# Performance work log

Hardware: AMD Instinct MI355X
Metric: run time of the kernel (lower is better)

Reference implementation:

```python
import jax, jax.numpy as jnp
import numpy as np

B, T, D = 2, 4096, 2048
HK, HV = 16, 32            # key heads, value heads (gqa_factor = 2)
AK, UV = 128, 128          # key head dim A, value head dim U
KEY_DIM = HK * AK          # 2048
VALUE_DIM = HV * UV        # 4096
CONV_DIM = 2 * KEY_DIM + VALUE_DIM  # 8192
KCONV = 4
CHUNK = 64
EPS = 1e-6


def setup_inputs() -> dict:
    key = jax.random.key(0)
    ks = jax.random.split(key, 10)
    s = lambda d: 1.0 / np.sqrt(d)
    return {
        "hidden": jax.random.normal(ks[0], (B, T, D), jnp.float32),
        "W_qkv": jax.random.normal(ks[1], (D, CONV_DIM), jnp.float32) * s(D),
        "W_z": jax.random.normal(ks[2], (D, VALUE_DIM), jnp.float32) * s(D),
        "W_b": jax.random.normal(ks[3], (D, HV), jnp.float32) * s(D),
        "W_a": jax.random.normal(ks[4], (D, HV), jnp.float32) * s(D),
        "conv_weight": jax.random.normal(ks[5], (CONV_DIM, KCONV), jnp.float32) * s(KCONV),
        "dt_bias": jnp.ones((HV,), jnp.float32),
        "A_log": jnp.log(jax.random.uniform(ks[6], (HV,), jnp.float32) * 16.0 + 1e-4),
        "norm_w": jnp.ones((UV,), jnp.float32),
        "W_out": jax.random.normal(ks[7], (VALUE_DIM, D), jnp.float32) * s(VALUE_DIM),
    }


def _l2norm(x, eps=1e-6):
    return x * jax.lax.rsqrt((x * x).sum(axis=-1, keepdims=True) + eps)


def _chunk_gated_delta_rule(q, k, v, g, beta, chunk_size=CHUNK):
    # inputs: q,k (B,T,Hv,A) l2-normalized below; v (B,T,Hv,U); g,beta (B,T,Hv)
    q = _l2norm(q)
    k = _l2norm(k)
    q, k, v = [x.transpose(0, 2, 1, 3).astype(jnp.float32) for x in (q, k, v)]
    beta = beta.transpose(0, 2, 1).astype(jnp.float32)
    g = g.transpose(0, 2, 1).astype(jnp.float32)
    Bs, H, Tt, A = k.shape
    U = v.shape[-1]
    pad = (chunk_size - Tt % chunk_size) % chunk_size
    if pad:
        q = jnp.pad(q, ((0, 0), (0, 0), (0, pad), (0, 0)))
        k = jnp.pad(k, ((0, 0), (0, 0), (0, pad), (0, 0)))
        v = jnp.pad(v, ((0, 0), (0, 0), (0, pad), (0, 0)))
        beta = jnp.pad(beta, ((0, 0), (0, 0), (0, pad)))
        g = jnp.pad(g, ((0, 0), (0, 0), (0, pad)))
    total = Tt + pad
    J = total // chunk_size
    q = q * (A ** -0.5)
    vb = v * beta[..., None]
    kb = k * beta[..., None]
    rs = lambda x, d: x.reshape(Bs, H, J, chunk_size, d)
    qj, kj, kbj = rs(q, A), rs(k, A), rs(kb, A)
    vbj = rs(vb, U)
    gj = jnp.cumsum(g.reshape(Bs, H, J, chunk_size), axis=-1)
    tril = jnp.tril(jnp.ones((chunk_size, chunk_size), jnp.float32))
    decay = jnp.exp((gj[..., :, None] - gj[..., None, :]) * tril) * tril
    upper = jnp.triu(jnp.ones((chunk_size, chunk_size), bool))
    attn = -(jnp.einsum('BHJLA,BHJMA->BHJLM', kbj, kj) * decay)
    attn = jnp.where(upper, 0.0, attn)

    def correction_step(i, a):  # sequential UT transform over rows
        row = a[..., i, :]
        return a.at[..., i, :].set(row + jnp.einsum('...j,...jk->...k', row, a))

    attn = jax.lax.fori_loop(1, chunk_size, correction_step, attn)
    attn = attn + jnp.eye(chunk_size, dtype=jnp.float32)
    v_corr = jnp.einsum('BHJLM,BHJMU->BHJLU', attn, vbj)
    k_cd = jnp.einsum('BHJLM,BHJMA->BHJLA', attn, kbj * jnp.exp(gj)[..., None])
    upper1 = jnp.triu(jnp.ones((chunk_size, chunk_size), bool), k=1)

    def chunk_step(st, j):  # st: (B,H,A,U) recurrent state
        qc, kc = qj[:, :, j], kj[:, :, j]
        vc, gc, kcd = v_corr[:, :, j], gj[:, :, j], k_cd[:, :, j]
        dm = decay[:, :, j]
        intra = jnp.einsum('BHLA,BHMA->BHLM', qc, kc) * dm
        intra = jnp.where(upper1, 0.0, intra)
        v_new = vc - jnp.einsum('BHLA,BHAU->BHLU', kcd, st)
        inter = jnp.exp(gc)[..., None] * jnp.einsum('BHLA,BHAU->BHLU', qc, st)
        out_c = inter + jnp.einsum('BHLM,BHMU->BHLU', intra, v_new)
        k_dec = kc * jnp.exp(gc[:, :, -1:] - gc)[..., None]
        st = st * jnp.exp(gc[:, :, -1])[..., None, None] + jnp.einsum('BHMA,BHMU->BHAU', k_dec, v_new)
        return st, out_c

    st0 = jnp.zeros((Bs, H, A, U), jnp.float32)
    _, outs = jax.lax.scan(chunk_step, st0, jnp.arange(J))
    out = outs.transpose(1, 2, 0, 3, 4).reshape(Bs, H, total, U)[:, :, :Tt]
    return out.transpose(0, 2, 1, 3)  # (B,T,H,U)


def _forward(hidden, W_qkv, W_z, W_b, W_a, conv_weight, dt_bias, A_log, norm_w, W_out):
    Bs, Tl, _ = hidden.shape
    mixed = (hidden @ W_qkv).transpose(0, 2, 1)  # (B, C, T)
    z = hidden @ W_z                              # (B, T, value_dim)
    b = hidden @ W_b                              # (B, T, Hv)
    a = hidden @ W_a                              # (B, T, Hv)
    # causal depthwise conv1d (kernel KCONV) + SiLU
    xp = jnp.pad(mixed, ((0, 0), (0, 0), (KCONV - 1, 0)))
    conv = sum(conv_weight[None, :, kk:kk + 1] * xp[:, :, kk:kk + Tl] for kk in range(KCONV))
    mixed = jax.nn.silu(conv).transpose(0, 2, 1)  # (B, T, C)
    q, k, v = jnp.split(mixed, [KEY_DIM, 2 * KEY_DIM], axis=-1)
    q = q.reshape(Bs, Tl, HK, AK)
    k = k.reshape(Bs, Tl, HK, AK)
    v = v.reshape(Bs, Tl, HV, UV)
    beta = jax.nn.sigmoid(b)
    g = -jnp.exp(A_log.astype(jnp.float32)) * jax.nn.softplus(a.astype(jnp.float32) + dt_bias)
    gqa = HV // HK
    q = jnp.repeat(q, gqa, axis=2)  # matches broadcast_to+reshape interleaving
    k = jnp.repeat(k, gqa, axis=2)
    core = _chunk_gated_delta_rule(q, k, v, g, beta)  # (B,T,Hv,U)
    # gated RMSNorm per value head (Mamba2/Qwen3-Next style: gate then norm)
    x = core.reshape(-1, UV)
    zf = z.reshape(-1, UV).astype(jnp.float32)
    xg = x * jax.nn.silu(zf)
    normed = norm_w * (xg * jax.lax.rsqrt((xg * xg).mean(-1, keepdims=True) + EPS))
    return normed.reshape(Bs, Tl, VALUE_DIM).astype(hidden.dtype) @ W_out


def reference(hidden, W_qkv, W_z, W_b, W_a, conv_weight, dt_bias, A_log, norm_w, W_out):
    return _forward(hidden, W_qkv, W_z, W_b, W_a, conv_weight, dt_bias, A_log, norm_w, W_out)
```

## Files before the change

kernel.cpp:

```cpp
#include <hip/hip_runtime.h>

#define B_   2
#define T_   4096
#define D_   2048
#define HV_  32
#define AK_  128
#define UV_  128
#define KD_  2048
#define VD_  4096
#define CD_  8192
#define CHK  64
#define NCH  (T_/CHK)

typedef __attribute__((ext_vector_type(4))) float  f32x4;
typedef __attribute__((ext_vector_type(8))) short  short8;
typedef __attribute__((ext_vector_type(4))) short  short4b;
typedef __attribute__((ext_vector_type(8))) unsigned short u16x8;
typedef __attribute__((ext_vector_type(4))) unsigned short u16x4;

__device__ __forceinline__ float bf2f(unsigned short u) {
  return __uint_as_float(((unsigned)u) << 16);
}
__device__ __forceinline__ unsigned short f2bf(float f) {
  unsigned u = __float_as_uint(f);
  return (unsigned short)((u + 0x7fffu + ((u >> 16) & 1u)) >> 16);
}
__device__ __forceinline__ void gload16(const void* g, void* l) {
  __builtin_amdgcn_global_load_lds((const __attribute__((address_space(1))) void*)g,
                                   (__attribute__((address_space(3))) void*)l, 16, 0, 0);
}

__global__ __launch_bounds__(256) void k_transpose(const float* __restrict__ src,
                                                   unsigned short* __restrict__ dst,
                                                   int K, int N) {
  __shared__ float tile[32][33];
  int k0 = blockIdx.x * 32, n0 = blockIdx.y * 32;
  int tx = threadIdx.x, ty = threadIdx.y;
  #pragma unroll
  for (int i = 0; i < 32; i += 8)
    tile[ty + i][tx] = src[(size_t)(k0 + ty + i) * N + n0 + tx];
  __syncthreads();
  #pragma unroll
  for (int i = 0; i < 32; i += 8)
    dst[(size_t)(n0 + ty + i) * K + k0 + tx] = f2bf(tile[tx][ty + i]);
}

__device__ __forceinline__ void storeC(float* p, float v) { *p = v; }
__device__ __forceinline__ void storeC(unsigned short* p, float v) { *p = f2bf(v); }

template <bool AGL, typename CT>
__global__ __launch_bounds__(256, 2) void k_gemm(const void* __restrict__ Av,
                                                 const unsigned short* __restrict__ BT,
                                                 CT* __restrict__ C, int N, int K) {
  __shared__ __attribute__((aligned(16))) short As[128 * 64];
  __shared__ __attribute__((aligned(16))) short Bs[256 * 64];
  const int tid  = threadIdx.x;
  const int bid  = blockIdx.x;
  const int tb   = bid & 63;
  const size_t bm = (size_t)(8 * (tb & 7) + (tb >> 3)) * 128;
  const size_t bn = (size_t)(bid >> 6) * 256;
  const int lane = tid & 63;
  const int wave = tid >> 6;
  const int wm = (wave >> 1) * 64;
  const int wn = (wave & 1) * 64;
  const int fr = lane & 15;
  const int kg = lane >> 4;
  const int lr = lane >> 3, lc8 = (lane & 7) * 8;
  const short* gb = (const short*)BT + (bn + wave * 64 + lr) * (size_t)K + lc8;
  short* lB = &Bs[wave * 64 * 64];
  const short* gab = (const short*)Av + (bm + wave * 32 + lr) * (size_t)K + lc8;
  short* lA = &As[wave * 32 * 64];

  f32x4 acc[4][8];
  #pragma unroll
  for (int i = 0; i < 4; ++i)
    #pragma unroll
    for (int j2 = 0; j2 < 8; ++j2) acc[i][j2] = (f32x4){0.f, 0.f, 0.f, 0.f};

  for (int kt = 0; kt < K; kt += 64) {
    __syncthreads();
    #pragma unroll
    for (int p = 0; p < 8; ++p)
      gload16(gb + kt + (size_t)(8 * p) * K, lB + (8 * p) * 64);
    if constexpr (AGL) {
      #pragma unroll
      for (int p = 0; p < 4; ++p)
        gload16(gab + kt + (size_t)(8 * p) * K, lA + (8 * p) * 64);
    } else {
      const float* Ag = (const float*)Av + bm * (size_t)K;
      #pragma unroll
      for (int s = 0; s < 8; ++s) {
        int ch = s * 256 + tid;
        int r = ch >> 4, c4 = (ch & 15) * 4;
        float4 v = *(const float4*)(Ag + (size_t)r * K + kt + c4);
        short4b sv = { (short)f2bf(v.x), (short)f2bf(v.y), (short)f2bf(v.z), (short)f2bf(v.w) };
        *(short4b*)&As[r * 64 + c4] = sv;
      }
    }
    __syncthreads();
    #pragma unroll
    for (int kk = 0; kk < 2; ++kk) {
      short8 af[4], bfr[8];
      #pragma unroll
      for (int mi = 0; mi < 4; ++mi) af[mi] = *(const short8*)&As[(wm + mi*16 + fr)*64 + kk*32 + kg*8];
      #pragma unroll
      for (int ni = 0; ni < 4; ++ni) {
        bfr[ni]     = *(const short8*)&Bs[(wn + ni*16 + fr)*64 + kk*32 + kg*8];
        bfr[4 + ni] = *(const short8*)&Bs[(128 + wn + ni*16 + fr)*64 + kk*32 + kg*8];
      }
      #pragma unroll
      for (int mi = 0; mi < 4; ++mi)
        #pragma unroll
        for (int ni = 0; ni < 8; ++ni)
          acc[mi][ni] = __builtin_amdgcn_mfma_f32_16x16x32_bf16(af[mi], bfr[ni], acc[mi][ni], 0, 0, 0);
    }
  }
  #pragma unroll
  for (int mi = 0; mi < 4; ++mi)
    #pragma unroll
    for (int ni = 0; ni < 8; ++ni) {
      size_t row = bm + wm + mi * 16 + kg * 4;
      size_t col = bn + (ni >= 4 ? 128 : 0) + wn + (ni & 3) * 16 + fr;
      #pragma unroll
      for (int e = 0; e < 4; ++e) storeC(&C[(row + e) * (size_t)N + col], acc[mi][ni][e]);
    }
}

__global__ __launch_bounds__(256) void k_beta_g(const float* __restrict__ hidden,
                                                const float* __restrict__ Wb,
                                                const float* __restrict__ Wa,
                                                const float* __restrict__ dt_bias,
                                                const float* __restrict__ A_log,
                                                float* __restrict__ betab,
                                                float* __restrict__ gbuf,
                                                unsigned short* __restrict__ hidb) {
  const int tid = threadIdx.x;
  const int r = tid >> 5, hh = tid & 31;
  const size_t bt = (size_t)blockIdx.x * 8 + r;
  const float* hrow = hidden + bt * D_;
  float sb = 0.f, sa = 0.f;
  for (int d = 0; d < D_; ++d) {
    float hv = hrow[d];
    sb += hv * Wb[d * 32 + hh];
    sa += hv * Wa[d * 32 + hh];
  }
  unsigned short* hb = hidb + bt * D_ + hh * 64;
  #pragma unroll
  for (int d2 = 0; d2 < 64; d2 += 8) {
    float4 v0 = *(const float4*)(hrow + hh * 64 + d2);
    float4 v1 = *(const float4*)(hrow + hh * 64 + d2 + 4);
    u16x8 o = { f2bf(v0.x), f2bf(v0.y), f2bf(v0.z), f2bf(v0.w),
                f2bf(v1.x), f2bf(v1.y), f2bf(v1.z), f2bf(v1.w) };
    *(u16x8*)(hb + d2) = o;
  }
  float beta = 1.f / (1.f + __expf(-sb));
  float xg = sa + dt_bias[hh];
  float sp = (xg > 20.f) ? xg : log1pf(__expf(xg));
  float g = -__expf(A_log[hh]) * sp;
  int b = (int)(bt >> 12);
  int t = (int)(bt & (T_ - 1));
  size_t o = ((size_t)b * HV_ + hh) * T_ + t;
  betab[o] = beta;
  gbuf[o] = g;
}

__global__ __launch_bounds__(256) void k_qkv(const unsigned short* __restrict__ mqk,
                                             const float* __restrict__ cw,
                                             unsigned short* __restrict__ qn,
                                             unsigned short* __restrict__ kn) {
  const int row = blockIdx.x;
  const int b = row >> 12, t = row & (T_ - 1);
  const int tid = threadIdx.x;
  const int c0 = tid * 16;
  float4 w[16];
  #pragma unroll
  for (int e = 0; e < 16; ++e) w[e] = *(const float4*)&cw[(size_t)(c0 + e) * 4];
  float acc[16];
  #pragma unroll
  for (int e = 0; e < 16; ++e) acc[e] = 0.f;
  #pragma unroll
  for (int p = 0; p < 4; ++p) {
    int ts = t - 3 + p;
    if (ts < 0) continue;
    const unsigned short* src = mqk + (size_t)(b * T_ + ts) * 4096 + c0;
    u16x8 v0 = *(const u16x8*)src;
    u16x8 v1 = *(const u16x8*)(src + 8);
    #pragma unroll
    for (int e = 0; e < 8; ++e) {
      acc[e]     += bf2f(v0[e]) * ((const float*)&w[e])[p];
      acc[8 + e] += bf2f(v1[e]) * ((const float*)&w[8 + e])[p];
    }
  }
  float s = 0.f;
  #pragma unroll
  for (int e = 0; e < 16; ++e) {
    float x = acc[e];
    x = x / (1.f + __expf(-x));
    acc[e] = x;
    s += x * x;
  }
  s += __shfl_xor(s, 1); s += __shfl_xor(s, 2); s += __shfl_xor(s, 4);
  float sc = rsqrtf(s + 1e-6f);
  bool isq = (c0 < KD_);
  if (isq) sc *= 0.08838834764831845f;
  int ch = isq ? c0 : (c0 - KD_);
  int hk = ch >> 7, cc = ch & 127;
  unsigned short* dst = (isq ? qn : kn) + ((size_t)(b * 16 + hk) * T_ + t) * 128 + cc;
  u16x8 o0, o1;
  #pragma unroll
  for (int e = 0; e < 8; ++e) { o0[e] = f2bf(acc[e] * sc); o1[e] = f2bf(acc[8 + e] * sc); }
  *(u16x8*)dst = o0;
  *(u16x8*)(dst + 8) = o1;
}

__global__ __launch_bounds__(256) void k_prep(const unsigned short* __restrict__ kn,
                                              const float* __restrict__ gbuf,
                                              const float* __restrict__ betab,
                                              unsigned short* __restrict__ Tg,
                                              unsigned short* __restrict__ knT,
                                              float* __restrict__ gjc) {
  __shared__ __attribute__((aligned(16))) unsigned short kl[CHK][136];
  __shared__ float L[CHK][65];
  __shared__ float W1[CHK][65];
  __shared__ float gj[CHK], bet[CHK];
  const int tid = threadIdx.x;
  const int blk = blockIdx.x;
  const int j = blk & 63, h = (blk >> 6) & 31, b = blk >> 11;
  const int hk = h >> 1;
  const int t0 = j * CHK;
  const int lane = tid & 63, wv = tid >> 6;
  const int fr = lane & 15, kg = lane >> 4;
  const int ty = tid >> 4, tx = tid & 15;

  const unsigned short* ksrc = kn + ((size_t)(b * 16 + hk) * T_ + t0) * 128;
  #pragma unroll
  for (int p = 0; p < 4; ++p) {
    int id = p * 256 + tid;
    int r = id >> 4, c = (id & 15) * 8;
    *(u16x8*)&kl[r][c] = *(const u16x8*)(ksrc + (size_t)r * 128 + c);
  }
  if (tid < 64) {
    float gval = gbuf[((size_t)b * HV_ + h) * T_ + t0 + tid];
    #pragma unroll
    for (int off = 1; off < 64; off <<= 1) {
      float o = __shfl_up(gval, off);
      if (tid >= off) gval += o;
    }
    gj[tid] = gval;
    gjc[((size_t)(b * HV_ + h) * NCH + j) * 64 + tid] = gval;
    bet[tid] = betab[((size_t)b * HV_ + h) * T_ + t0 + tid];
  }
  __syncthreads();

  if ((h & 1) == 0) {
    unsigned short* kd = knT + ((size_t)(b * 16 + hk) * NCH + j) * 8192;
    int a = tid >> 1, l0 = (tid & 1) * 32;
    u16x8 o[4];
    #pragma unroll
    for (int i = 0; i < 32; ++i) ((unsigned short*)o)[i] = kl[l0 + i][a];
    #pragma unroll
    for (int p = 0; p < 4; ++p) *(u16x8*)(kd + a * 64 + l0 + p * 8) = o[p];
  }

  {
    const int s0 = 16 * wv;
    f32x4 ag[4];
    #pragma unroll
    for (int mt = 0; mt < 4; ++mt) ag[mt] = (f32x4){0.f, 0.f, 0.f, 0.f};
    #pragma unroll
    for (int ks = 0; ks < 4; ++ks) {
      short8 af = *(const short8*)&kl[s0 + fr][ks * 32 + kg * 8];
      #pragma unroll
      for (int mt = 0; mt < 4; ++mt) {
        short8 bfv = *(const short8*)&kl[mt * 16 + fr][ks * 32 + kg * 8];
        ag[mt] = __builtin_amdgcn_mfma_f32_16x16x32_bf16(af, bfv, ag[mt], 0, 0, 0);
      }
    }
    #pragma unroll
    for (int mt = 0; mt < 4; ++mt)
      #pragma unroll
      for (int e = 0; e < 4; ++e) {
        int l = s0 + kg * 4 + e, m = mt * 16 + fr;
        L[l][m] = (l > m) ? (-bet[l] * ag[mt][e] * __expf(gj[l] - gj[m])) : 0.f;
      }
  }
  __syncthreads();
  for (int i = tid; i < CHK * CHK; i += 256) { int l = i >> 6, m = i & 63; W1[l][m] = L[l][m]; }
  __syncthreads();

  #pragma unroll
  for (int dk = 1; dk <= 5; ++dk) {
    const int p2 = 1 << (dk - 1);
    float s4[4][4];
    #pragma unroll
    for (int i = 0; i < 4; ++i)
      #pragma unroll
      for (int c = 0; c < 4; ++c) s4[i][c] = 0.f;
    {
      const int hi = 16 * wv + 15 - p2;
      for (int jm = p2; jm <= hi; ++jm) {
        float wl[4], wr[4];
        #pragma unroll
        for (int i = 0; i < 4; ++i) wl[i] = W1[ty * 4 + i][jm];
        #pragma unroll
        for (int c = 0; c < 4; ++c) wr[c] = W1[jm][tx * 4 + c];
        #pragma unroll
        for (int i = 0; i < 4; ++i)
          #pragma unroll
          for (int c = 0; c < 4; ++c) s4[i][c] += wl[i] * wr[c];
      }
    }
    __syncthreads();
    #pragma unroll
    for (int i = 0; i < 4; ++i)
      #pragma unroll
      for (int c = 0; c < 4; ++c) W1[ty * 4 + i][tx * 4 + c] = s4[i][c];
    __syncthreads();
    float pu[4][4];
    #pragma unroll
    for (int i = 0; i < 4; ++i)
      #pragma unroll
      for (int c = 0; c < 4; ++c) pu[i][c] = L[ty * 4 + i][tx * 4 + c] + W1[ty * 4 + i][tx * 4 + c];
    {
      const int hi = 16 * wv + 14;
      for (int jm = p2 * 2; jm <= hi; ++jm) {
        float pl[4], wr[4];
        #pragma unroll
        for (int i = 0; i < 4; ++i) pl[i] = L[ty * 4 + i][jm];
        #pragma unroll
        for (int c = 0; c < 4; ++c) wr[c] = W1[jm][tx * 4 + c];
        #pragma unroll
        for (int i = 0; i < 4; ++i)
          #pragma unroll
          for (int c = 0; c < 4; ++c) pu[i][c] += pl[i] * wr[c];
      }
    }
    __syncthreads();
    #pragma unroll
    for (int i = 0; i < 4; ++i)
      #pragma unroll
      for (int c = 0; c < 4; ++c) L[ty * 4 + i][tx * 4 + c] = pu[i][c];
    __syncthreads();
  }
  unsigned short* td = Tg + (size_t)blk * 4096;
  #pragma unroll
  for (int pp = 0; pp < 2; ++pp) {
    int id = pp * 256 + tid;
    int l = id >> 3, m8 = (id & 7) * 8;
    u16x8 o;
    #pragma unroll
    for (int e = 0; e < 8; ++e) {
      float v = L[l][m8 + e] + ((l == m8 + e) ? 1.f : 0.f);
      o[e] = f2bf(v);
    }
    *(u16x8*)(td + (size_t)l * 64 + m8) = o;
  }
}

__global__ __launch_bounds__(256) void k_scan(const unsigned short* __restrict__ qn,
                                              const unsigned short* __restrict__ kn,
                                              const unsigned short* __restrict__ mv,
                                              const unsigned short* __restrict__ Tg,
                                              const unsigned short* __restrict__ knT,
                                              const float* __restrict__ gjc,
                                              const float* __restrict__ betab,
                                              const float* __restrict__ cw,
                                              unsigned short* __restrict__ xout) {
  __shared__ __attribute__((aligned(16))) unsigned short kl[CHK][136], ql[CHK][136];
  __shared__ __attribute__((aligned(16))) unsigned short Ubuf[9216];
  __shared__ float ST[16][132];
  __shared__ __attribute__((aligned(16))) unsigned short SbT[16][136];
  __shared__ __attribute__((aligned(16))) unsigned short vbT[16][72], vnT[16][72], vndT[16][72];
  __shared__ float gj[CHK], bet[CHK], eg[CHK], edec[CHK], beg[CHK];

  unsigned short (*Tl)[72]   = (unsigned short(*)[72])(&Ubuf[0]);
  unsigned short (*intr)[72] = (unsigned short(*)[72])(&Ubuf[4608]);

  const int tid = threadIdx.x;
  const int blk = blockIdx.x;
  const int xcd  = blk & 7;
  const int slot = blk >> 3;
  const int g    = xcd + 8 * (slot >> 4);
  const int wgrp = slot & 15;
  const int b  = g >> 4;
  const int hk = g & 15;
  const int h  = hk * 2 + (wgrp >> 3);
  const int us = wgrp & 7;
  const int u0 = us * 16;
  const int lane = tid & 63, wv = tid >> 6;
  const int fr = lane & 15, kg = lane >> 4;
  const int s0 = 16 * wv;

  const int cvl = tid >> 2, c4 = (tid & 3) * 4;
  float4 wv4[4];
  #pragma unroll
  for (int i = 0; i < 4; ++i)
    wv4[i] = *(const float4*)&cw[(size_t)(2 * KD_ + h * 128 + u0 + c4 + i) * 4];

  for (int i = tid; i < 16 * 132; i += 256) (&ST[0][0])[i] = 0.f;

  const unsigned short* qsrc = qn + (size_t)(b * 16 + hk) * T_ * 128;
  const unsigned short* ksrc = kn + (size_t)(b * 16 + hk) * T_ * 128;
  const unsigned short* tsrc = Tg + (size_t)((b * 32 + h) * 64) * 4096;
  const unsigned short* knsrc = knT + (size_t)(b * 16 + hk) * NCH * 8192;
  const float* gsrc = gjc + (size_t)(b * 32 + h) * 4096;
  const float* bsrc = betab + ((size_t)b * HV_ + h) * T_;

  const int rr = tid >> 4, cc8 = (tid & 15) * 8;
  const int tr = tid >> 3, tc8 = (tid & 7) * 8;

  u16x8 krg[4], qrg[4], trg[2];
  u16x4 vld[4];
  float g_r = 0.f, b_r = 0.f;

  #pragma unroll
  for (int p = 0; p < 4; ++p) {
    int r = p * 16 + rr;
    krg[p] = *(const u16x8*)(ksrc + (size_t)r * 128 + cc8);
    qrg[p] = *(const u16x8*)(qsrc + (size_t)r * 128 + cc8);
  }
  #pragma unroll
  for (int p = 0; p < 2; ++p) {
    int r = p * 32 + tr;
    trg[p] = *(const u16x8*)(tsrc + (size_t)r * 64 + tc8);
  }
  if (tid < 64) { g_r = gsrc[tid]; b_r = bsrc[tid]; }
  #pragma unroll
  for (int p = 0; p < 4; ++p) {
    int ts = cvl - 3 + p;
    vld[p] = (ts >= 0) ? *(const u16x4*)(mv + (size_t)(b * T_ + ts) * 4096 + h * 128 + u0 + c4)
                       : (u16x4){0, 0, 0, 0};
  }
  #pragma unroll
  for (int p = 0; p < 4; ++p) {
    int r = p * 16 + rr;
    *(u16x8*)&kl[r][cc8] = krg[p];
    *(u16x8*)&ql[r][cc8] = qrg[p];
  }
  #pragma unroll
  for (int p = 0; p < 2; ++p) {
    int r = p * 32 + tr;
    *(u16x8*)&Tl[r][tc8] = trg[p];
  }
  if (tid < 64) { gj[tid] = g_r; bet[tid] = b_r; }
  __syncthreads();

  for (int j = 0; j < NCH; ++j) {
    const int t0 = j * CHK;
    short8 kr[2][2];
    #pragma unroll
    for (int t2 = 0; t2 < 2; ++t2) {
      int a0 = wv * 32 + t2 * 16;
      #pragma unroll
      for (int ks = 0; ks < 2; ++ks)
        kr[t2][ks] = *(const short8*)(knsrc + (size_t)j * 8192 + (a0 + fr) * 64 + ks * 32 + kg * 8);
    }
    if (j + 1 < NCH) {
      const int t1 = t0 + CHK;
      #pragma unroll
      for (int p = 0; p < 4; ++p) {
        int r = p * 16 + rr;
        krg[p] = *(const u16x8*)(ksrc + (size_t)(t1 + r) * 128 + cc8);
        qrg[p] = *(const u16x8*)(qsrc + (size_t)(t1 + r) * 128 + cc8);
      }
      #pragma unroll
      for (int p = 0; p < 2; ++p) {
        int r = p * 32 + tr;
        trg[p] = *(const u16x8*)(tsrc + (size_t)(j + 1) * 4096 + r * 64 + tc8);
      }
      if (tid < 64) { g_r = gsrc[(j + 1) * 64 + tid]; b_r = bsrc[t1 + tid]; }
    }
    if (tid < 64) {
      float gl = gj[63];
      float e = __expf(gj[tid]);
      eg[tid] = e;
      edec[tid] = __expf(gl - gj[tid]);
      beg[tid] = bet[tid] * e;
    }
    {
      float a4[4] = {0.f, 0.f, 0.f, 0.f};
      #pragma unroll
      for (int p = 0; p < 4; ++p)
        #pragma unroll
        for (int i = 0; i < 4; ++i) a4[i] += bf2f(vld[p][i]) * ((const float*)&wv4[i])[p];
      float be = bet[cvl];
      #pragma unroll
      for (int i = 0; i < 4; ++i) {
        float x = a4[i];
        x = x / (1.f + __expf(-x)) * be;
        vbT[c4 + i][cvl] = f2bf(x);
      }
    }
    if (j + 1 < NCH) {
      #pragma unroll
      for (int p = 0; p < 4; ++p) {
        int ts = t0 + CHK + cvl - 3 + p;
        vld[p] = *(const u16x4*)(mv + (size_t)(b * T_ + ts) * 4096 + h * 128 + u0 + c4);
      }
    }
    {
      int u = tid >> 4, a8 = (tid & 15) * 8;
      u16x8 o;
      #pragma unroll
      for (int e = 0; e < 8; ++e) o[e] = f2bf(ST[u][a8 + e]);
      *(u16x8*)&SbT[u][a8] = o;
    }
    __syncthreads();

    {
      f32x4 ag[4];
      #pragma unroll
      for (int mt = 0; mt < 4; ++mt) ag[mt] = (f32x4){0.f, 0.f, 0.f, 0.f};
      #pragma unroll
      for (int ks = 0; ks < 4; ++ks) {
        short8 af = *(const short8*)&ql[s0 + fr][ks * 32 + kg * 8];
        #pragma unroll
        for (int mt = 0; mt < 4; ++mt) {
          short8 bfv = *(const short8*)&kl[mt * 16 + fr][ks * 32 + kg * 8];
          ag[mt] = __builtin_amdgcn_mfma_f32_16x16x32_bf16(af, bfv, ag[mt], 0, 0, 0);
        }
      }
      #pragma unroll
      for (int mt = 0; mt < 4; ++mt)
        #pragma unroll
        for (int e = 0; e < 4; ++e) {
          int l = s0 + kg * 4 + e, m = mt * 16 + fr;
          float v = (l >= m) ? (ag[mt][e] * __expf(gj[l] - gj[m])) : 0.f;
          intr[l][m] = f2bf(v);
        }
    }
    {
      f32x4 a1 = (f32x4){0.f, 0.f, 0.f, 0.f};
      #pragma unroll
      for (int ks = 0; ks < 4; ++ks) {
        short8 af = *(const short8*)&kl[s0 + fr][ks * 32 + kg * 8];
        short8 bfv = *(const short8*)&SbT[fr][ks * 32 + kg * 8];
        a1 = __builtin_amdgcn_mfma_f32_16x16x32_bf16(af, bfv, a1, 0, 0, 0);
      }
      #pragma unroll
      for (int e = 0; e < 4; ++e) {
        int l = s0 + kg * 4 + e;
        float vm = bf2f(vbT[fr][l]) - beg[l] * a1[e];
        vbT[fr][l] = f2bf(vm);
      }
    }
    __syncthreads();
    {
      f32x4 a2 = (f32x4){0.f, 0.f, 0.f, 0.f};
      #pragma unroll
      for (int ks = 0; ks < 2; ++ks) {
        short8 af = *(const short8*)&Tl[s0 + fr][ks * 32 + kg * 8];
        short8 bfv = *(const short8*)&vbT[fr][ks * 32 + kg * 8];
        a2 = __builtin_amdgcn_mfma_f32_16x16x32_bf16(af, bfv, a2, 0, 0, 0);
      }
      #pragma unroll
      for (int e = 0; e < 4; ++e) {
        int l = s0 + kg * 4 + e;
        vnT[fr][l]  = f2bf(a2[e]);
        vndT[fr][l] = f2bf(a2[e] * edec[l]);
      }
    }
    __syncthreads();
    {
      f32x4 ai = (f32x4){0.f, 0.f, 0.f, 0.f};
      f32x4 aq = (f32x4){0.f, 0.f, 0.f, 0.f};
      #pragma unroll
      for (int ks = 0; ks < 2; ++ks) {
        short8 af = *(const short8*)&intr[s0 + fr][ks * 32 + kg * 8];
        short8 bfv = *(const short8*)&vnT[fr][ks * 32 + kg * 8];
        ai = __builtin_amdgcn_mfma_f32_16x16x32_bf16(af, bfv, ai, 0, 0, 0);
      }
      #pragma unroll
      for (int ks = 0; ks < 4; ++ks) {
        short8 af = *(const short8*)&ql[s0 + fr][ks * 32 + kg * 8];
        short8 bfv = *(const short8*)&SbT[fr][ks * 32 + kg * 8];
        aq = __builtin_amdgcn_mfma_f32_16x16x32_bf16(af, bfv, aq, 0, 0, 0);
      }
      #pragma unroll
      for (int e = 0; e < 4; ++e) {
        int l = s0 + kg * 4 + e;
        float o = eg[l] * aq[e] + ai[e];
        xout[((size_t)(b * T_ + t0 + l) * HV_ + h) * UV_ + u0 + fr] = f2bf(o);
      }
    }
    {
      float egl = eg[63];
      #pragma unroll
      for (int t2 = 0; t2 < 2; ++t2) {
        int a0 = wv * 32 + t2 * 16;
        f32x4 cf;
        #pragma unroll
        for (int e = 0; e < 4; ++e) cf[e] = ST[kg * 4 + e][a0 + fr] * egl;
        #pragma unroll
        for (int ks = 0; ks < 2; ++ks) {
          short8 af = *(const short8*)&vndT[fr][ks * 32 + kg * 8];
          cf = __builtin_amdgcn_mfma_f32_16x16x32_bf16(af, kr[t2][ks], cf, 0, 0, 0);
        }
        #pragma unroll
        for (int e = 0; e < 4; ++e) ST[kg * 4 + e][a0 + fr] = cf[e];
      }
    }
    __syncthreads();
    if (j + 1 < NCH) {
      #pragma unroll
      for (int p = 0; p < 4; ++p) {
        int r = p * 16 + rr;
        *(u16x8*)&kl[r][cc8] = krg[p];
        *(u16x8*)&ql[r][cc8] = qrg[p];
      }
      #pragma unroll
      for (int p = 0; p < 2; ++p) {
        int r = p * 32 + tr;
        *(u16x8*)&Tl[r][tc8] = trg[p];
      }
      if (tid < 64) { gj[tid] = g_r; bet[tid] = b_r; }
    }
    __syncthreads();
  }
}

__global__ __launch_bounds__(256) void k_gate_norm(const unsigned short* __restrict__ x,
                                                   const unsigned short* __restrict__ z,
                                                   const float* __restrict__ nw,
                                                   unsigned short* __restrict__ out) {
  const int row = blockIdx.x * 4 + (threadIdx.x >> 6);
  const int lane = threadIdx.x & 63;
  const unsigned short* xp = x + (size_t)row * UV_;
  const unsigned short* zp = z + (size_t)row * UV_;
  float x0 = bf2f(xp[lane]), x1 = bf2f(xp[lane + 64]);
  float z0 = bf2f(zp[lane]), z1 = bf2f(zp[lane + 64]);
  float g0 = x0 * (z0 / (1.f + __expf(-z0)));
  float g1 = x1 * (z1 / (1.f + __expf(-z1)));
  float s = g0 * g0 + g1 * g1;
  #pragma unroll
  for (int off = 32; off > 0; off >>= 1) s += __shfl_xor(s, off);
  float r = rsqrtf(s * (1.f / UV_) + 1e-6f);
  out[(size_t)row * UV_ + lane]      = f2bf(nw[lane] * g0 * r);
  out[(size_t)row * UV_ + lane + 64] = f2bf(nw[lane + 64] * g1 * r);
}

extern "C" void kernel_launch(void* const* d_in, const int* in_sizes, int n_in,
                              void* d_out, int out_size, void* d_ws, size_t ws_size,
                              hipStream_t stream) {
  (void)in_sizes; (void)n_in; (void)out_size; (void)ws_size;
  const float* hidden  = (const float*)d_in[0];
  const float* W_qkv   = (const float*)d_in[1];
  const float* W_z     = (const float*)d_in[2];
  const float* W_b     = (const float*)d_in[3];
  const float* W_a     = (const float*)d_in[4];
  const float* conv_w  = (const float*)d_in[5];
  const float* dt_bias = (const float*)d_in[6];
  const float* A_log   = (const float*)d_in[7];
  const float* norm_w  = (const float*)d_in[8];
  const float* W_out   = (const float*)d_in[9];
  float* out = (float*)d_out;

  const size_t MB = 1048576ull;
  char* w = (char*)d_ws;
  unsigned short* wqkvT = (unsigned short*)(w);
  unsigned short* Tg    = (unsigned short*)(w);
  unsigned short* mqk   = (unsigned short*)(w + 32 * MB);
  unsigned short* xcore = (unsigned short*)(w + 32 * MB);
  unsigned short* mv    = (unsigned short*)(w + 96 * MB);
  unsigned short* normed= (unsigned short*)(w + 96 * MB);
  unsigned short* hidb  = (unsigned short*)(w + 160 * MB);
  unsigned short* qn    = (unsigned short*)(w + 160 * MB);
  unsigned short* zb    = (unsigned short*)(w + 160 * MB);
  unsigned short* knT   = (unsigned short*)(w + 192 * MB);
  unsigned short* kn    = (unsigned short*)(w + 224 * MB);
  unsigned short* wzT   = (unsigned short*)(w + 224 * MB);
  unsigned short* woutT = (unsigned short*)(w + 240 * MB);
  float*          betab = (float*)(w + 288 * MB);
  float*          gbuf  = (float*)(w + 289 * MB);
  float*          gjc   = (float*)(w + 290 * MB);

  k_beta_g<<<dim3(B_ * T_ / 8), 256, 0, stream>>>(hidden, W_b, W_a, dt_bias, A_log, betab, gbuf, hidb);
  k_transpose<<<dim3(D_ / 32, CD_ / 32), dim3(32, 8), 0, stream>>>(W_qkv, wqkvT, D_, CD_);
  k_gemm<true, unsigned short><<<dim3(64 * 16), 256, 0, stream>>>(hidb, wqkvT, mqk, 4096, 2048);
  k_gemm<true, unsigned short><<<dim3(64 * 16), 256, 0, stream>>>(hidb, wqkvT + (size_t)4096 * 2048, mv, 4096, 2048);
  k_qkv<<<dim3(B_ * T_), 256, 0, stream>>>(mqk, conv_w, qn, kn);
  k_prep<<<dim3(B_ * HV_ * NCH), 256, 0, stream>>>(kn, gbuf, betab, Tg, knT, gjc);
  k_scan<<<dim3(B_ * HV_ * 8), 256, 0, stream>>>(qn, kn, mv, Tg, knT, gjc, betab, conv_w, xcore);
  k_transpose<<<dim3(D_ / 32, VD_ / 32), dim3(32, 8), 0, stream>>>(W_z, wzT, D_, VD_);
  k_gemm<false, unsigned short><<<dim3(64 * 16), 256, 0, stream>>>(hidden, wzT, zb, 4096, 2048);
  k_transpose<<<dim3(VD_ / 32, D_ / 32), dim3(32, 8), 0, stream>>>(W_out, woutT, VD_, D_);
  k_gate_norm<<<dim3(B_ * T_ * HV_ / 4), 256, 0, stream>>>(xcore, zb, norm_w, normed);
  k_gemm<true, float><<<dim3(64 * 8), 256, 0, stream>>>(normed, woutT, out, 2048, 4096);
}
```

Before: 1.628 ms.

## Vectorize beta/g projection via transposed weights; load scan Q and T fragments directly

Adds a small f32 transpose of W_b and W_a so the beta/g projection kernel reads contiguous float4 rows of hidden and weights instead of strided scalar loads. In the scan kernel, the q and T chunk tiles are no longer staged through shared memory; each wave loads its MFMA fragments straight from global memory every chunk. This cuts LDS usage and the register prefetch path, but the q/T loads now sit on the critical path of each chunk iteration instead of being prefetched a chunk ahead.

```diff
diff --git a/kernel.cpp b/kernel.cpp
--- a/kernel.cpp
+++ b/kernel.cpp
@@ -43,6 +43,21 @@
   #pragma unroll
   for (int i = 0; i < 32; i += 8)
     dst[(size_t)(n0 + ty + i) * K + k0 + tx] = f2bf(tile[tx][ty + i]);
+}
+
+__global__ __launch_bounds__(256) void k_transpose_f32(const float* __restrict__ src,
+                                                       float* __restrict__ dst,
+                                                       int K, int N) {
+  __shared__ float tile[32][33];
+  int k0 = blockIdx.x * 32, n0 = blockIdx.y * 32;
+  int tx = threadIdx.x, ty = threadIdx.y;
+  #pragma unroll
+  for (int i = 0; i < 32; i += 8)
+    tile[ty + i][tx] = src[(size_t)(k0 + ty + i) * N + n0 + tx];
+  __syncthreads();
+  #pragma unroll
+  for (int i = 0; i < 32; i += 8)
+    dst[(size_t)(n0 + ty + i) * K + k0 + tx] = tile[tx][ty + i];
 }
 
 __device__ __forceinline__ void storeC(float* p, float v) { *p = v; }
@@ -127,8 +142,7 @@
 }
 
 __global__ __launch_bounds__(256) void k_beta_g(const float* __restrict__ hidden,
-                                                const float* __restrict__ Wb,
-                                                const float* __restrict__ Wa,
+                                                const float* __restrict__ wbaT,
                                                 const float* __restrict__ dt_bias,
                                                 const float* __restrict__ A_log,
                                                 float* __restrict__ betab,
@@ -138,11 +152,15 @@
   const int r = tid >> 5, hh = tid & 31;
   const size_t bt = (size_t)blockIdx.x * 8 + r;
   const float* hrow = hidden + bt * D_;
+  const float* wb = wbaT + (size_t)hh * 2048;
+  const float* wa = wbaT + (size_t)(32 + hh) * 2048;
   float sb = 0.f, sa = 0.f;
-  for (int d = 0; d < D_; ++d) {
-    float hv = hrow[d];
-    sb += hv * Wb[d * 32 + hh];
-    sa += hv * Wa[d * 32 + hh];
+  for (int d = 0; d < D_; d += 4) {
+    float4 h4 = *(const float4*)(hrow + d);
+    float4 b4 = *(const float4*)(wb + d);
+    float4 a4 = *(const float4*)(wa + d);
+    sb += h4.x * b4.x; sb += h4.y * b4.y; sb += h4.z * b4.z; sb += h4.w * b4.w;
+    sa += h4.x * a4.x; sa += h4.y * a4.y; sa += h4.z * a4.z; sa += h4.w * a4.w;
   }
   unsigned short* hb = hidb + bt * D_ + hh * 64;
   #pragma unroll
@@ -366,15 +384,12 @@
                                               const float* __restrict__ betab,
                                               const float* __restrict__ cw,
                                               unsigned short* __restrict__ xout) {
-  __shared__ __attribute__((aligned(16))) unsigned short kl[CHK][136], ql[CHK][136];
-  __shared__ __attribute__((aligned(16))) unsigned short Ubuf[9216];
+  __shared__ __attribute__((aligned(16))) unsigned short kl[CHK][136];
+  __shared__ __attribute__((aligned(16))) unsigned short intr[CHK][72];
   __shared__ float ST[16][132];
   __shared__ __attribute__((aligned(16))) unsigned short SbT[16][136];
   __shared__ __attribute__((aligned(16))) unsigned short vbT[16][72], vnT[16][72], vndT[16][72];
   __shared__ float gj[CHK], bet[CHK], eg[CHK], edec[CHK], beg[CHK];
-
-  unsigned short (*Tl)[72]   = (unsigned short(*)[72])(&Ubuf[0]);
-  unsigned short (*intr)[72] = (unsigned short(*)[72])(&Ubuf[4608]);
 
   const int tid = threadIdx.x;
   const int blk = blockIdx.x;
@@ -407,9 +422,8 @@
   const float* bsrc = betab + ((size_t)b * HV_ + h) * T_;
 
   const int rr = tid >> 4, cc8 = (tid & 15) * 8;
-  const int tr = tid >> 3, tc8 = (tid & 7) * 8;
-
-  u16x8 krg[4], qrg[4], trg[2];
+
+  u16x8 krg[4];
   u16x4 vld[4];
   float g_r = 0.f, b_r = 0.f;
 
@@ -417,12 +431,6 @@
   for (int p = 0; p < 4; ++p) {
     int r = p * 16 + rr;
     krg[p] = *(const u16x8*)(ksrc + (size_t)r * 128 + cc8);
-    qrg[p] = *(const u16x8*)(qsrc + (size_t)r * 128 + cc8);
-  }
-  #pragma unroll
-  for (int p = 0; p < 2; ++p) {
-    int r = p * 32 + tr;
-    trg[p] = *(const u16x8*)(tsrc + (size_t)r * 64 + tc8);
   }
   if (tid < 64) { g_r = gsrc[tid]; b_r = bsrc[tid]; }
   #pragma unroll
@@ -435,19 +443,13 @@
   for (int p = 0; p < 4; ++p) {
     int r = p * 16 + rr;
     *(u16x8*)&kl[r][cc8] = krg[p];
-    *(u16x8*)&ql[r][cc8] = qrg[p];
-  }
-  #pragma unroll
-  for (int p = 0; p < 2; ++p) {
-    int r = p * 32 + tr;
-    *(u16x8*)&Tl[r][tc8] = trg[p];
   }
   if (tid < 64) { gj[tid] = g_r; bet[tid] = b_r; }
   __syncthreads();
 
   for (int j = 0; j < NCH; ++j) {
     const int t0 = j * CHK;
-    short8 kr[2][2];
+    short8 kr[2][2], qf[4], tf[2];
     #pragma unroll
     for (int t2 = 0; t2 < 2; ++t2) {
       int a0 = wv * 32 + t2 * 16;
@@ -455,18 +457,18 @@
       for (int ks = 0; ks < 2; ++ks)
         kr[t2][ks] = *(const short8*)(knsrc + (size_t)j * 8192 + (a0 + fr) * 64 + ks * 32 + kg * 8);
     }
+    #pragma unroll
+    for (int ks = 0; ks < 4; ++ks)
+      qf[ks] = *(const short8*)(qsrc + (size_t)(t0 + s0 + fr) * 128 + ks * 32 + kg * 8);
+    #pragma unroll
+    for (int ks = 0; ks < 2; ++ks)
+      tf[ks] = *(const short8*)(tsrc + (size_t)j * 4096 + (s0 + fr) * 64 + ks * 32 + kg * 8);
     if (j + 1 < NCH) {
       const int t1 = t0 + CHK;
       #pragma unroll
       for (int p = 0; p < 4; ++p) {
         int r = p * 16 + rr;
         krg[p] = *(const u16x8*)(ksrc + (size_t)(t1 + r) * 128 + cc8);
-        qrg[p] = *(const u16x8*)(qsrc + (size_t)(t1 + r) * 128 + cc8);
-      }
-      #pragma unroll
-      for (int p = 0; p < 2; ++p) {
-        int r = p * 32 + tr;
-        trg[p] = *(const u16x8*)(tsrc + (size_t)(j + 1) * 4096 + r * 64 + tc8);
       }
       if (tid < 64) { g_r = gsrc[(j + 1) * 64 + tid]; b_r = bsrc[t1 + tid]; }
     }
@@ -513,11 +515,10 @@
       for (int mt = 0; mt < 4; ++mt) ag[mt] = (f32x4){0.f, 0.f, 0.f, 0.f};
       #pragma unroll
       for (int ks = 0; ks < 4; ++ks) {
-        short8 af = *(const short8*)&ql[s0 + fr][ks * 32 + kg * 8];
         #pragma unroll
         for (int mt = 0; mt < 4; ++mt) {
           short8 bfv = *(const short8*)&kl[mt * 16 + fr][ks * 32 + kg * 8];
-          ag[mt] = __builtin_amdgcn_mfma_f32_16x16x32_bf16(af, bfv, ag[mt], 0, 0, 0);
+          ag[mt] = __builtin_amdgcn_mfma_f32_16x16x32_bf16(qf[ks], bfv, ag[mt], 0, 0, 0);
         }
       }
       #pragma unroll
@@ -549,9 +550,8 @@
       f32x4 a2 = (f32x4){0.f, 0.f, 0.f, 0.f};
       #pragma unroll
       for (int ks = 0; ks < 2; ++ks) {
-        short8 af = *(const short8*)&Tl[s0 + fr][ks * 32 + kg * 8];
         short8 bfv = *(const short8*)&vbT[fr][ks * 32 + kg * 8];
-        a2 = __builtin_amdgcn_mfma_f32_16x16x32_bf16(af, bfv, a2, 0, 0, 0);
+        a2 = __builtin_amdgcn_mfma_f32_16x16x32_bf16(tf[ks], bfv, a2, 0, 0, 0);
       }
       #pragma unroll
       for (int e = 0; e < 4; ++e) {
@@ -572,9 +572,8 @@
       }
       #pragma unroll
       for (int ks = 0; ks < 4; ++ks) {
-        short8 af = *(const short8*)&ql[s0 + fr][ks * 32 + kg * 8];
         short8 bfv = *(const short8*)&SbT[fr][ks * 32 + kg * 8];
-        aq = __builtin_amdgcn_mfma_f32_16x16x32_bf16(af, bfv, aq, 0, 0, 0);
+        aq = __builtin_amdgcn_mfma_f32_16x16x32_bf16(qf[ks], bfv, aq, 0, 0, 0);
       }
       #pragma unroll
       for (int e = 0; e < 4; ++e) {
@@ -606,12 +605,6 @@
       for (int p = 0; p < 4; ++p) {
         int r = p * 16 + rr;
         *(u16x8*)&kl[r][cc8] = krg[p];
-        *(u16x8*)&ql[r][cc8] = qrg[p];
-      }
-      #pragma unroll
-      for (int p = 0; p < 2; ++p) {
-        int r = p * 32 + tr;
-        *(u16x8*)&Tl[r][tc8] = trg[p];
       }
       if (tid < 64) { gj[tid] = g_r; bet[tid] = b_r; }
     }
@@ -659,6 +652,7 @@
   char* w = (char*)d_ws;
   unsigned short* wqkvT = (unsigned short*)(w);
   unsigned short* Tg    = (unsigned short*)(w);
+  float*          wbaT  = (float*)(w + 32 * MB);
   unsigned short* mqk   = (unsigned short*)(w + 32 * MB);
   unsigned short* xcore = (unsigned short*)(w + 32 * MB);
   unsigned short* mv    = (unsigned short*)(w + 96 * MB);
@@ -674,7 +668,9 @@
   float*          gbuf  = (float*)(w + 289 * MB);
   float*          gjc   = (float*)(w + 290 * MB);
 
-  k_beta_g<<<dim3(B_ * T_ / 8), 256, 0, stream>>>(hidden, W_b, W_a, dt_bias, A_log, betab, gbuf, hidb);
+  k_transpose_f32<<<dim3(D_ / 32, 1), dim3(32, 8), 0, stream>>>(W_b, wbaT, D_, 32);
+  k_transpose_f32<<<dim3(D_ / 32, 1), dim3(32, 8), 0, stream>>>(W_a, wbaT + 32 * 2048, D_, 32);
+  k_beta_g<<<dim3(B_ * T_ / 8), 256, 0, stream>>>(hidden, wbaT, dt_bias, A_log, betab, gbuf, hidb);
   k_transpose<<<dim3(D_ / 32, CD_ / 32), dim3(32, 8), 0, stream>>>(W_qkv, wqkvT, D_, CD_);
   k_gemm<true, unsigned short><<<dim3(64 * 16), 256, 0, stream>>>(hidb, wqkvT, mqk, 4096, 2048);
   k_gemm<true, unsigned short><<<dim3(64 * 16), 256, 0, stream>>>(hidb, wqkvT + (size_t)4096 * 2048, mv, 4096, 2048);
```

After: 1.878 ms. 15.4% more time.
